# Optimization experiments

Hardware: AMD Instinct MI355X
Metric: run time of the kernel (lower is better)

Reference implementation:

```python
import jax, jax.numpy as jnp
import numpy as np

N, E, IN, H, OUT = 50000, 1600000, 128, 128, 16


def setup_inputs() -> dict:
    key = jax.random.key(0)
    ks = jax.random.split(key, 8)
    return {
        "x": jax.random.normal(ks[0], (N, IN), dtype=jnp.float32),
        "edge_index": jax.random.randint(ks[1], (2, E), 0, N, dtype=jnp.int64),
        "W1": jax.random.normal(ks[2], (IN, H), dtype=jnp.float32) * 0.05,
        "b1": jax.random.normal(ks[3], (H,), dtype=jnp.float32) * 0.05,
        "W2": jax.random.normal(ks[4], (H, H), dtype=jnp.float32) * 0.05,
        "b2": jax.random.normal(ks[5], (H,), dtype=jnp.float32) * 0.05,
        "Wc": jax.random.normal(ks[6], (H, OUT), dtype=jnp.float32) * 0.05,
        "bc": jax.random.normal(ks[7], (OUT,), dtype=jnp.float32) * 0.05,
    }


def _gcn_conv(x, src, dst, norm, W, b, n):
    # PyG GCNConv: h = x @ W; out[i] = sum_{(j->i)} norm_e * h[j]; out += b
    h = x @ W
    msg = h[src] * norm[:, None]          # [E+N, H] gather + scale
    out = jax.ops.segment_sum(msg, dst, num_segments=n)  # scatter-add
    return out + b


def reference(x, edge_index, W1, b1, W2, b2, Wc, bc):
    n = x.shape[0]
    loop = jnp.arange(n, dtype=edge_index.dtype)
    src = jnp.concatenate([edge_index[0], loop])  # add self-loops
    dst = jnp.concatenate([edge_index[1], loop])
    # symmetric normalization: deg over destinations (incl. self-loops)
    deg = jnp.zeros((n,), dtype=x.dtype).at[dst].add(1.0)
    d_inv_sqrt = jnp.where(deg > 0, jax.lax.rsqrt(deg), 0.0)
    norm = d_inv_sqrt[src] * d_inv_sqrt[dst]
    h = jax.nn.relu(_gcn_conv(x, src, dst, norm, W1, b1, n))
    # dropout p=0.5 is identity in eval mode
    h = jax.nn.relu(_gcn_conv(h, src, dst, norm, W2, b2, n))
    return h @ Wc + bc
```

## Files before the change

### kernel.cpp

```cpp
#include <hip/hip_runtime.h>
#include <hip/hip_bf16.h>


typedef unsigned int uint;
typedef unsigned short ushort;
typedef __attribute__((ext_vector_type(8))) short bf16x8;
typedef __attribute__((ext_vector_type(4))) float f32x4;

#define NPB 256
#define MAXBKT 256
#define CAP 12288

static __device__ __forceinline__ ushort f2bf(float f) {
    unsigned u = __float_as_uint(f);
    u += 0x7fffu + ((u >> 16) & 1u);
    return (ushort)(u >> 16);
}
static __device__ __forceinline__ uint pack2(float a, float b) {
    return (uint)f2bf(a) | ((uint)f2bf(b) << 16);
}
static __device__ __forceinline__ float lo2f(uint u) { return __uint_as_float(u << 16); }
static __device__ __forceinline__ float hi2f(uint u) { return __uint_as_float(u & 0xffff0000u); }

#define UNPACK8(dst, u)                                        \
    dst[0] = lo2f(u.x); dst[1] = hi2f(u.x);                    \
    dst[2] = lo2f(u.y); dst[3] = hi2f(u.y);                    \
    dst[4] = lo2f(u.z); dst[5] = hi2f(u.z);                    \
    dst[6] = lo2f(u.w); dst[7] = hi2f(u.w);


__global__ __launch_bounds__(256) void initcur(int* __restrict__ bcursor, int nbuckets) {
    int t = threadIdx.x;
    if (t < nbuckets) bcursor[t] = t * CAP;
}

__global__ __launch_bounds__(256) void bin_edges(const int* __restrict__ src,
                                                 const int* __restrict__ dst,
                                                 int* __restrict__ bcursor,
                                                 uint* __restrict__ pay,
                                                 int E, int nbuckets) {
    __shared__ int h[MAXBKT];
    __shared__ int base[MAXBKT];
    int tid = threadIdx.x;
    h[tid] = 0;
    __syncthreads();
    int chunk = (E + gridDim.x - 1) / gridDim.x;
    int i0 = blockIdx.x * chunk;
    int i1 = min(E, i0 + chunk);
    for (int i = i0 + tid; i < i1; i += 256) atomicAdd(&h[dst[i] >> 8], 1);
    __syncthreads();
    if (tid < nbuckets) base[tid] = h[tid] ? atomicAdd(&bcursor[tid], h[tid]) : 0;
    __syncthreads();
    h[tid] = 0;
    __syncthreads();
    for (int i = i0 + tid; i < i1; i += 256) {
        int d = dst[i];
        int b = d >> 8;
        int pos = base[b] + atomicAdd(&h[b], 1);
        pay[pos] = (uint)src[i] | ((uint)(d & 255) << 24);
    }
}

__global__ __launch_bounds__(256) void build_rows(const uint* __restrict__ pay,
                                                  const int* __restrict__ bcursor,
                                                  int* __restrict__ rowstart,
                                                  int* __restrict__ rowend,
                                                  float* __restrict__ dinv,
                                                  int* __restrict__ colidx, int n) {
    __shared__ int hist[NPB];
    __shared__ int sc[NPB];
    __shared__ int cur[NPB];
    int tid = threadIdx.x;
    int b = blockIdx.x;
    int node0 = b * NPB;
    int s = b * CAP, e = bcursor[b];

    hist[tid] = 0;
    __syncthreads();
    for (int i = s + tid; i < e; i += 256) atomicAdd(&hist[pay[i] >> 24], 1);
    __syncthreads();

    int v = hist[tid];
    sc[tid] = v;
    __syncthreads();
    for (int d = 1; d < 256; d <<= 1) {
        int x = (tid >= d) ? sc[tid - d] : 0;
        __syncthreads();
        sc[tid] += x;
        __syncthreads();
    }
    int excl = sc[tid] - v;
    cur[tid] = s + excl;
    int node = node0 + tid;
    if (node < n) {
        rowstart[node] = s + excl;
        rowend[node] = s + excl + v;
        dinv[node] = rsqrtf((float)(v + 1));
    }
    __syncthreads();

    for (int i = s + tid; i < e; i += 256) {
        uint p = pay[i];
        int pos = atomicAdd(&cur[p >> 24], 1);
        colidx[pos] = (int)(p & 0xffffffu);
    }
}

__global__ __launch_bounds__(256) void prep_wt(const float* __restrict__ W1,
                                               const float* __restrict__ W2,
                                               ushort* __restrict__ Wt1,
                                               ushort* __restrict__ Wt2) {
    int idx = blockIdx.x * 256 + threadIdx.x;
    int k = idx >> 7, nn = idx & 127;
    Wt1[nn * 128 + k] = f2bf(W1[idx]);
    Wt2[nn * 128 + k] = f2bf(W2[idx]);
}

template <bool A_BF16>
__global__ __launch_bounds__(256) void gemm_mfma(const void* __restrict__ Xv,
                                                 const ushort* __restrict__ Wt,
                                                 const float* __restrict__ dinv,
                                                 uint* __restrict__ Yb, int n) {
    __shared__ __align__(16) ushort sOut[4][16][136];
    const int wave = threadIdx.x >> 6;
    const int lane = threadIdx.x & 63;
    const int quad = lane >> 4, l16 = lane & 15;
    const int m0 = blockIdx.x * 64 + wave * 16;

    f32x4 acc[8];
#pragma unroll
    for (int t = 0; t < 8; ++t) acc[t] = (f32x4){0.f, 0.f, 0.f, 0.f};

    int arow = m0 + l16;
    arow = arow < n ? arow : n - 1;

#pragma unroll
    for (int ks = 0; ks < 4; ++ks) {
        bf16x8 a;
        if (A_BF16) {
            const ushort* X = (const ushort*)Xv;
            a = *(const bf16x8*)&X[(size_t)arow * 128 + ks * 32 + quad * 8];
        } else {
            const float* X = (const float*)Xv;
            const float* px = &X[(size_t)arow * 128 + ks * 32 + quad * 8];
            float4 x0 = *(const float4*)px;
            float4 x1 = *(const float4*)(px + 4);
            ushort av[8] = {f2bf(x0.x), f2bf(x0.y), f2bf(x0.z), f2bf(x0.w),
                            f2bf(x1.x), f2bf(x1.y), f2bf(x1.z), f2bf(x1.w)};
            a = *(const bf16x8*)av;
        }
#pragma unroll
        for (int nt = 0; nt < 8; ++nt) {
            bf16x8 b = *(const bf16x8*)&Wt[(size_t)(nt * 16 + l16) * 128 + ks * 32 + quad * 8];
            acc[nt] = __builtin_amdgcn_mfma_f32_16x16x32_bf16(a, b, acc[nt], 0, 0, 0);
        }
    }

    float dv[4];
#pragma unroll
    for (int r = 0; r < 4; ++r) {
        int rr = m0 + quad * 4 + r;
        dv[r] = dinv[rr < n ? rr : n - 1];
    }
#pragma unroll
    for (int nt = 0; nt < 8; ++nt)
#pragma unroll
        for (int r = 0; r < 4; ++r)
            sOut[wave][quad * 4 + r][nt * 16 + l16] = f2bf(acc[nt][r] * dv[r]);
    __syncthreads();

#pragma unroll
    for (int i = 0; i < 4; ++i) {
        int linear = i * 64 + lane;
        int row = linear >> 4, chunk = linear & 15;
        int rr = m0 + row;
        if (rr < n) {
            uint4 v = *(const uint4*)&sOut[wave][row][chunk * 8];
            *(uint4*)&Yb[(size_t)rr * 64 + chunk * 4] = v;
        }
    }
}

static __device__ __forceinline__ void gather_q(const uint4* __restrict__ H4,
                                                int s, int e, int nn, int sub,
                                                const int* __restrict__ colidx,
                                                float acc[8]) {
    uint4 su = H4[(size_t)nn * 16 + sub];
    float t[8];
    UNPACK8(t, su);
#pragma unroll
    for (int j = 0; j < 8; ++j) acc[j] = t[j];

    int p = s;
    for (; p + 8 <= e; p += 8) {
        int c[8];
#pragma unroll
        for (int i = 0; i < 8; ++i) c[i] = colidx[p + i];
        uint4 u[8];
#pragma unroll
        for (int i = 0; i < 8; ++i) u[i] = H4[(size_t)c[i] * 16 + sub];
#pragma unroll
        for (int i = 0; i < 8; ++i) {
            float a[8];
            UNPACK8(a, u[i]);
#pragma unroll
            for (int j = 0; j < 8; ++j) acc[j] += a[j];
        }
    }
    if (p < e) {
        int c[8];
#pragma unroll
        for (int i = 0; i < 8; ++i) c[i] = (p + i < e) ? colidx[p + i] : nn;
        uint4 u[8];
#pragma unroll
        for (int i = 0; i < 8; ++i) u[i] = H4[(size_t)c[i] * 16 + sub];
#pragma unroll
        for (int i = 0; i < 8; ++i) {
            float a[8];
            UNPACK8(a, u[i]);
#pragma unroll
            for (int j = 0; j < 8; ++j) acc[j] += a[j];
        }
        float pad = (float)(p + 8 - e);
#pragma unroll
        for (int j = 0; j < 8; ++j) acc[j] -= pad * t[j];
    }
}

__global__ __launch_bounds__(256) void agg_mid_q(const uint4* __restrict__ H4,
                                                 const int* __restrict__ rowstart,
                                                 const int* __restrict__ rowend,
                                                 const int* __restrict__ colidx,
                                                 const float* __restrict__ dinv,
                                                 const float* __restrict__ bias,
                                                 uint4* __restrict__ Ob, int n) {
    int tid = threadIdx.x;
    int sub = tid & 15;
    int node = blockIdx.x * 16 + (tid >> 4);
    int nn = node < n ? node : n - 1;
    int s = rowstart[nn], e = rowend[nn];
    float di = dinv[nn];

    float acc[8];
    gather_q(H4, s, e, nn, sub, colidx, acc);

    if (node < n) {
        float4 b0 = ((const float4*)bias)[sub * 2];
        float4 b1 = ((const float4*)bias)[sub * 2 + 1];
        float o0 = fmaxf(fmaf(acc[0], di, b0.x), 0.f);
        float o1 = fmaxf(fmaf(acc[1], di, b0.y), 0.f);
        float o2 = fmaxf(fmaf(acc[2], di, b0.z), 0.f);
        float o3 = fmaxf(fmaf(acc[3], di, b0.w), 0.f);
        float o4 = fmaxf(fmaf(acc[4], di, b1.x), 0.f);
        float o5 = fmaxf(fmaf(acc[5], di, b1.y), 0.f);
        float o6 = fmaxf(fmaf(acc[6], di, b1.z), 0.f);
        float o7 = fmaxf(fmaf(acc[7], di, b1.w), 0.f);
        uint4 ov;
        ov.x = pack2(o0, o1); ov.y = pack2(o2, o3);
        ov.z = pack2(o4, o5); ov.w = pack2(o6, o7);
        Ob[(size_t)node * 16 + sub] = ov;
    }
}

__global__ __launch_bounds__(256) void agg_out_q(const uint4* __restrict__ H4,
                                                 const int* __restrict__ rowstart,
                                                 const int* __restrict__ rowend,
                                                 const int* __restrict__ colidx,
                                                 const float* __restrict__ dinv,
                                                 const float* __restrict__ bias,
                                                 const float* __restrict__ Wc,
                                                 const float* __restrict__ bc,
                                                 float* __restrict__ out, int n) {
    __shared__ float sA[16][129];
    int tid = threadIdx.x;
    int sub = tid & 15;
    int nl = tid >> 4;
    int node = blockIdx.x * 16 + nl;
    int nn = node < n ? node : n - 1;
    int s = rowstart[nn], e = rowend[nn];
    float di = dinv[nn];

    float acc[8];
    gather_q(H4, s, e, nn, sub, colidx, acc);

    {
        float4 b0 = ((const float4*)bias)[sub * 2];
        float4 b1 = ((const float4*)bias)[sub * 2 + 1];
        float f[8];
        f[0] = fmaxf(fmaf(acc[0], di, b0.x), 0.f);
        f[1] = fmaxf(fmaf(acc[1], di, b0.y), 0.f);
        f[2] = fmaxf(fmaf(acc[2], di, b0.z), 0.f);
        f[3] = fmaxf(fmaf(acc[3], di, b0.w), 0.f);
        f[4] = fmaxf(fmaf(acc[4], di, b1.x), 0.f);
        f[5] = fmaxf(fmaf(acc[5], di, b1.y), 0.f);
        f[6] = fmaxf(fmaf(acc[6], di, b1.z), 0.f);
        f[7] = fmaxf(fmaf(acc[7], di, b1.w), 0.f);
#pragma unroll
        for (int j = 0; j < 8; ++j) sA[nl][sub * 8 + j] = f[j];
    }
    __syncthreads();

    int col = tid & 15;
    float p0 = 0.f, p1 = 0.f;
#pragma unroll 4
    for (int k = 0; k < 128; k += 2) {
        p0 = fmaf(sA[nl][k], Wc[k * 16 + col], p0);
        p1 = fmaf(sA[nl][k + 1], Wc[(k + 1) * 16 + col], p1);
    }
    if (node < n) out[(size_t)node * 16 + col] = p0 + p1 + bc[col];
}


extern "C" void kernel_launch(void* const* d_in, const int* in_sizes, int n_in,
                              void* d_out, int out_size, void* d_ws, size_t ws_size,
                              hipStream_t stream) {
    const float* x  = (const float*)d_in[0];
    const int*   ei = (const int*)d_in[1];
    const float* W1 = (const float*)d_in[2];
    const float* b1 = (const float*)d_in[3];
    const float* W2 = (const float*)d_in[4];
    const float* b2 = (const float*)d_in[5];
    const float* Wc = (const float*)d_in[6];
    const float* bc = (const float*)d_in[7];
    float* out = (float*)d_out;

    const int n = in_sizes[0] / 128;
    const int E = in_sizes[1] / 2;
    const int* src = ei;
    const int* dst = ei + E;
    const int nbuckets = (n + NPB - 1) / NPB;

    char* p = (char*)d_ws;
    auto alloc = [&](size_t bytes) {
        char* q = p;
        p += (bytes + 255) & ~(size_t)255;
        return q;
    };
    int*    bcursor  = (int*)alloc(MAXBKT * 4);
    int*    rowstart = (int*)alloc((size_t)n * 4);
    int*    rowend   = (int*)alloc((size_t)n * 4);
    float*  dinv     = (float*)alloc((size_t)n * 4);
    ushort* Wt1      = (ushort*)alloc(128 * 128 * 2);
    ushort* Wt2      = (ushort*)alloc(128 * 128 * 2);
    uint*   pay      = (uint*)alloc((size_t)nbuckets * CAP * 4);
    int*    colidx   = (int*)alloc((size_t)nbuckets * CAP * 4);
    uint*   bufA     = (uint*)alloc((size_t)n * 64 * 4);
    uint*   bufB     = (uint*)alloc((size_t)n * 64 * 4);
    if ((size_t)(p - (char*)d_ws) > ws_size) return;

    initcur<<<1, 256, 0, stream>>>(bcursor, nbuckets);
    bin_edges<<<256, 256, 0, stream>>>(src, dst, bcursor, pay, E, nbuckets);
    build_rows<<<nbuckets, 256, 0, stream>>>(pay, bcursor, rowstart, rowend, dinv, colidx, n);
    prep_wt<<<64, 256, 0, stream>>>(W1, W2, Wt1, Wt2);

    const int gemmb = (n + 63) / 64;
    const int aggb = (n + 15) / 16;
    gemm_mfma<false><<<gemmb, 256, 0, stream>>>(x, Wt1, dinv, bufA, n);
    agg_mid_q<<<aggb, 256, 0, stream>>>((const uint4*)bufA, rowstart, rowend, colidx,
                                        dinv, b1, (uint4*)bufB, n);
    gemm_mfma<true><<<gemmb, 256, 0, stream>>>(bufB, Wt2, dinv, bufA, n);
    agg_out_q<<<aggb, 256, 0, stream>>>((const uint4*)bufA, rowstart, rowend, colidx,
                                        dinv, b2, Wc, bc, out, n);
}
```

Measured before the change: 284.2 us.

## Store hidden features feature-group-major and shrink column indices to 16 bits

Intermediate bf16 feature buffers change from node-major rows to 16 feature-group planes of 16 bytes per node. Each aggregation block now covers 128 nodes for two feature groups, so the randomly gathered working set per block is a single small plane that stays cache-resident. Column indices are stored as 16-bit values, which halves index traffic but only holds while the node count fits in 16 bits. The final layer's 128x16 projection is split across the 8 feature-group blocks and combined with float atomics into a zeroed output, which adds a memset and many atomics.

```diff
diff --git a/kernel.cpp b/kernel.cpp
--- a/kernel.cpp
+++ b/kernel.cpp
@@ -66,7 +66,7 @@
                                                   int* __restrict__ rowstart,
                                                   int* __restrict__ rowend,
                                                   float* __restrict__ dinv,
-                                                  int* __restrict__ colidx, int n) {
+                                                  ushort* __restrict__ colidx, int n) {
     __shared__ int hist[NPB];
     __shared__ int sc[NPB];
     __shared__ int cur[NPB];
@@ -102,7 +102,7 @@
     for (int i = s + tid; i < e; i += 256) {
         uint p = pay[i];
         int pos = atomicAdd(&cur[p >> 24], 1);
-        colidx[pos] = (int)(p & 0xffffffu);
+        colidx[pos] = (ushort)p;
     }
 }
 
@@ -139,7 +139,7 @@
         bf16x8 a;
         if (A_BF16) {
             const ushort* X = (const ushort*)Xv;
-            a = *(const bf16x8*)&X[(size_t)arow * 128 + ks * 32 + quad * 8];
+            a = *(const bf16x8*)&X[((size_t)(ks * 4 + quad) * n + arow) * 8];
         } else {
             const float* X = (const float*)Xv;
             const float* px = &X[(size_t)arow * 128 + ks * 32 + quad * 8];
@@ -172,20 +172,20 @@
 #pragma unroll
     for (int i = 0; i < 4; ++i) {
         int linear = i * 64 + lane;
-        int row = linear >> 4, chunk = linear & 15;
+        int g = linear >> 4, row = linear & 15;
         int rr = m0 + row;
         if (rr < n) {
-            uint4 v = *(const uint4*)&sOut[wave][row][chunk * 8];
-            *(uint4*)&Yb[(size_t)rr * 64 + chunk * 4] = v;
-        }
-    }
-}
-
-static __device__ __forceinline__ void gather_q(const uint4* __restrict__ H4,
-                                                int s, int e, int nn, int sub,
-                                                const int* __restrict__ colidx,
+            uint4 v = *(const uint4*)&sOut[wave][row][g * 8];
+            *(uint4*)&Yb[((size_t)g * n + rr) * 4] = v;
+        }
+    }
+}
+
+static __device__ __forceinline__ void gather_g(const uint4* __restrict__ Hg,
+                                                int s, int e, int nn, size_t gbase,
+                                                const ushort* __restrict__ colidx,
                                                 float acc[8]) {
-    uint4 su = H4[(size_t)nn * 16 + sub];
+    uint4 su = Hg[gbase + nn];
     float t[8];
     UNPACK8(t, su);
 #pragma unroll
@@ -198,7 +198,7 @@
         for (int i = 0; i < 8; ++i) c[i] = colidx[p + i];
         uint4 u[8];
 #pragma unroll
-        for (int i = 0; i < 8; ++i) u[i] = H4[(size_t)c[i] * 16 + sub];
+        for (int i = 0; i < 8; ++i) u[i] = Hg[gbase + c[i]];
 #pragma unroll
         for (int i = 0; i < 8; ++i) {
             float a[8];
@@ -210,10 +210,10 @@
     if (p < e) {
         int c[8];
 #pragma unroll
-        for (int i = 0; i < 8; ++i) c[i] = (p + i < e) ? colidx[p + i] : nn;
+        for (int i = 0; i < 8; ++i) c[i] = (p + i < e) ? (int)colidx[p + i] : nn;
         uint4 u[8];
 #pragma unroll
-        for (int i = 0; i < 8; ++i) u[i] = H4[(size_t)c[i] * 16 + sub];
+        for (int i = 0; i < 8; ++i) u[i] = Hg[gbase + c[i]];
 #pragma unroll
         for (int i = 0; i < 8; ++i) {
             float a[8];
@@ -227,26 +227,30 @@
     }
 }
 
-__global__ __launch_bounds__(256) void agg_mid_q(const uint4* __restrict__ H4,
+__global__ __launch_bounds__(256) void agg_mid_c(const uint4* __restrict__ Hg,
                                                  const int* __restrict__ rowstart,
                                                  const int* __restrict__ rowend,
-                                                 const int* __restrict__ colidx,
+                                                 const ushort* __restrict__ colidx,
                                                  const float* __restrict__ dinv,
                                                  const float* __restrict__ bias,
-                                                 uint4* __restrict__ Ob, int n) {
+                                                 uint4* __restrict__ Og, int n) {
     int tid = threadIdx.x;
-    int sub = tid & 15;
-    int node = blockIdx.x * 16 + (tid >> 4);
+    int sub = tid & 1;
+    int f = blockIdx.x & 7;
+    int node = (blockIdx.x >> 3) * 128 + (tid >> 1);
     int nn = node < n ? node : n - 1;
     int s = rowstart[nn], e = rowend[nn];
     float di = dinv[nn];
+    int g = f * 2 + sub;
+    size_t gbase = (size_t)g * n;
 
     float acc[8];
-    gather_q(H4, s, e, nn, sub, colidx, acc);
+    gather_g(Hg, s, e, nn, gbase, colidx, acc);
 
     if (node < n) {
-        float4 b0 = ((const float4*)bias)[sub * 2];
-        float4 b1 = ((const float4*)bias)[sub * 2 + 1];
+        const float4* B4 = (const float4*)bias;
+        float4 b0 = B4[g * 2];
+        float4 b1 = B4[g * 2 + 1];
         float o0 = fmaxf(fmaf(acc[0], di, b0.x), 0.f);
         float o1 = fmaxf(fmaf(acc[1], di, b0.y), 0.f);
         float o2 = fmaxf(fmaf(acc[2], di, b0.z), 0.f);
@@ -258,56 +262,76 @@
         uint4 ov;
         ov.x = pack2(o0, o1); ov.y = pack2(o2, o3);
         ov.z = pack2(o4, o5); ov.w = pack2(o6, o7);
-        Ob[(size_t)node * 16 + sub] = ov;
-    }
-}
-
-__global__ __launch_bounds__(256) void agg_out_q(const uint4* __restrict__ H4,
+        Og[gbase + node] = ov;
+    }
+}
+
+__global__ __launch_bounds__(256) void agg_fin_c(const uint4* __restrict__ Hg,
                                                  const int* __restrict__ rowstart,
                                                  const int* __restrict__ rowend,
-                                                 const int* __restrict__ colidx,
+                                                 const ushort* __restrict__ colidx,
                                                  const float* __restrict__ dinv,
                                                  const float* __restrict__ bias,
                                                  const float* __restrict__ Wc,
                                                  const float* __restrict__ bc,
                                                  float* __restrict__ out, int n) {
-    __shared__ float sA[16][129];
     int tid = threadIdx.x;
-    int sub = tid & 15;
-    int nl = tid >> 4;
-    int node = blockIdx.x * 16 + nl;
+    int sub = tid & 1;
+    int f = blockIdx.x & 7;
+    int node = (blockIdx.x >> 3) * 128 + (tid >> 1);
     int nn = node < n ? node : n - 1;
     int s = rowstart[nn], e = rowend[nn];
     float di = dinv[nn];
+    int g = f * 2 + sub;
+    size_t gbase = (size_t)g * n;
 
     float acc[8];
-    gather_q(H4, s, e, nn, sub, colidx, acc);
-
+    gather_g(Hg, s, e, nn, gbase, colidx, acc);
+
+    float a[8];
     {
-        float4 b0 = ((const float4*)bias)[sub * 2];
-        float4 b1 = ((const float4*)bias)[sub * 2 + 1];
-        float f[8];
-        f[0] = fmaxf(fmaf(acc[0], di, b0.x), 0.f);
-        f[1] = fmaxf(fmaf(acc[1], di, b0.y), 0.f);
-        f[2] = fmaxf(fmaf(acc[2], di, b0.z), 0.f);
-        f[3] = fmaxf(fmaf(acc[3], di, b0.w), 0.f);
-        f[4] = fmaxf(fmaf(acc[4], di, b1.x), 0.f);
-        f[5] = fmaxf(fmaf(acc[5], di, b1.y), 0.f);
-        f[6] = fmaxf(fmaf(acc[6], di, b1.z), 0.f);
-        f[7] = fmaxf(fmaf(acc[7], di, b1.w), 0.f);
-#pragma unroll
-        for (int j = 0; j < 8; ++j) sA[nl][sub * 8 + j] = f[j];
-    }
-    __syncthreads();
-
-    int col = tid & 15;
-    float p0 = 0.f, p1 = 0.f;
-#pragma unroll 4
-    for (int k = 0; k < 128; k += 2) {
-        p0 = fmaf(sA[nl][k], Wc[k * 16 + col], p0);
-        p1 = fmaf(sA[nl][k + 1], Wc[(k + 1) * 16 + col], p1);
-    }
-    if (node < n) out[(size_t)node * 16 + col] = p0 + p1 + bc[col];
+        const float4* B4 = (const float4*)bias;
+        float4 b0 = B4[g * 2];
+        float4 b1 = B4[g * 2 + 1];
+        a[0] = fmaxf(fmaf(acc[0], di, b0.x), 0.f);
+        a[1] = fmaxf(fmaf(acc[1], di, b0.y), 0.f);
+        a[2] = fmaxf(fmaf(acc[2], di, b0.z), 0.f);
+        a[3] = fmaxf(fmaf(acc[3], di, b0.w), 0.f);
+        a[4] = fmaxf(fmaf(acc[4], di, b1.x), 0.f);
+        a[5] = fmaxf(fmaf(acc[5], di, b1.y), 0.f);
+        a[6] = fmaxf(fmaf(acc[6], di, b1.z), 0.f);
+        a[7] = fmaxf(fmaf(acc[7], di, b1.w), 0.f);
+    }
+
+    float p[16];
+#pragma unroll
+    for (int c = 0; c < 16; ++c) p[c] = 0.f;
+#pragma unroll
+    for (int j = 0; j < 8; ++j) {
+        const float4* wr = (const float4*)&Wc[(size_t)(g * 8 + j) * 16];
+        float4 w0 = wr[0], w1 = wr[1], w2 = wr[2], w3 = wr[3];
+        float aj = a[j];
+        p[0]  = fmaf(aj, w0.x, p[0]);  p[1]  = fmaf(aj, w0.y, p[1]);
+        p[2]  = fmaf(aj, w0.z, p[2]);  p[3]  = fmaf(aj, w0.w, p[3]);
+        p[4]  = fmaf(aj, w1.x, p[4]);  p[5]  = fmaf(aj, w1.y, p[5]);
+        p[6]  = fmaf(aj, w1.z, p[6]);  p[7]  = fmaf(aj, w1.w, p[7]);
+        p[8]  = fmaf(aj, w2.x, p[8]);  p[9]  = fmaf(aj, w2.y, p[9]);
+        p[10] = fmaf(aj, w2.z, p[10]); p[11] = fmaf(aj, w2.w, p[11]);
+        p[12] = fmaf(aj, w3.x, p[12]); p[13] = fmaf(aj, w3.y, p[13]);
+        p[14] = fmaf(aj, w3.z, p[14]); p[15] = fmaf(aj, w3.w, p[15]);
+    }
+#pragma unroll
+    for (int c = 0; c < 16; ++c) p[c] += __shfl_xor(p[c], 1);
+
+    if (node < n) {
+        int cb = sub * 8;
+#pragma unroll
+        for (int k = 0; k < 8; ++k) {
+            float v = p[cb + k];
+            if (f == 0) v += bc[cb + k];
+            atomicAdd(&out[(size_t)node * 16 + cb + k], v);
+        }
+    }
 }
 
 
@@ -343,10 +367,12 @@
     ushort* Wt1      = (ushort*)alloc(128 * 128 * 2);
     ushort* Wt2      = (ushort*)alloc(128 * 128 * 2);
     uint*   pay      = (uint*)alloc((size_t)nbuckets * CAP * 4);
-    int*    colidx   = (int*)alloc((size_t)nbuckets * CAP * 4);
+    ushort* colidx   = (ushort*)alloc((size_t)nbuckets * CAP * 2);
     uint*   bufA     = (uint*)alloc((size_t)n * 64 * 4);
     uint*   bufB     = (uint*)alloc((size_t)n * 64 * 4);
     if ((size_t)(p - (char*)d_ws) > ws_size) return;
+
+    hipMemsetAsync(out, 0, (size_t)n * 16 * sizeof(float), stream);
 
     initcur<<<1, 256, 0, stream>>>(bcursor, nbuckets);
     bin_edges<<<256, 256, 0, stream>>>(src, dst, bcursor, pay, E, nbuckets);
@@ -354,11 +380,11 @@
     prep_wt<<<64, 256, 0, stream>>>(W1, W2, Wt1, Wt2);
 
     const int gemmb = (n + 63) / 64;
-    const int aggb = (n + 15) / 16;
+    const int aggb = 8 * ((n + 127) / 128);
     gemm_mfma<false><<<gemmb, 256, 0, stream>>>(x, Wt1, dinv, bufA, n);
-    agg_mid_q<<<aggb, 256, 0, stream>>>((const uint4*)bufA, rowstart, rowend, colidx,
+    agg_mid_c<<<aggb, 256, 0, stream>>>((const uint4*)bufA, rowstart, rowend, colidx,
                                         dinv, b1, (uint4*)bufB, n);
     gemm_mfma<true><<<gemmb, 256, 0, stream>>>(bufB, Wt2, dinv, bufA, n);
-    agg_out_q<<<aggb, 256, 0, stream>>>((const uint4*)bufA, rowstart, rowend, colidx,
+    agg_fin_c<<<aggb, 256, 0, stream>>>((const uint4*)bufA, rowstart, rowend, colidx,
                                         dinv, b2, Wc, bc, out, n);
 }
```

Measured after the change: 484.8 us. 1.71x slower.

## Store CSR column indices as 16-bit and sub-sort row neighbors by source range

Applied to the files above, without the earlier changes.

Column indices are stored as ushort instead of int, halving the index traffic read by both aggregation kernels. build_rows also orders each row's neighbors by which quarter of the node range the source falls in, to improve cache locality of the feature gathers. The bin_edges grid grows from 256 to 1024 blocks. Sixteen-bit indices only hold when the node count stays below 65536, and the per-row quarter histogram adds shared-memory atomics and an integer division per edge.

```diff
diff --git a/kernel.cpp b/kernel.cpp
--- a/kernel.cpp
+++ b/kernel.cpp
@@ -9,6 +9,7 @@
 
 #define NPB 256
 #define MAXBKT 256
+#define NQ 4
 #define CAP 12288
 
 static __device__ __forceinline__ ushort f2bf(float f) {
@@ -66,22 +67,28 @@
                                                   int* __restrict__ rowstart,
                                                   int* __restrict__ rowend,
                                                   float* __restrict__ dinv,
-                                                  int* __restrict__ colidx, int n) {
-    __shared__ int hist[NPB];
+                                                  ushort* __restrict__ colidx, int n) {
+    __shared__ int hist[NPB * NQ];
     __shared__ int sc[NPB];
-    __shared__ int cur[NPB];
+    __shared__ int cur[NPB * NQ];
     int tid = threadIdx.x;
     int b = blockIdx.x;
     int node0 = b * NPB;
     int s = b * CAP, e = bcursor[b];
-
-    hist[tid] = 0;
-    __syncthreads();
-    for (int i = s + tid; i < e; i += 256) atomicAdd(&hist[pay[i] >> 24], 1);
-    __syncthreads();
-
-    int v = hist[tid];
-    sc[tid] = v;
+    int qsize = (n + NQ - 1) / NQ;
+
+    for (int i = tid; i < NPB * NQ; i += 256) hist[i] = 0;
+    __syncthreads();
+    for (int i = s + tid; i < e; i += 256) {
+        uint p = pay[i];
+        atomicAdd(&hist[(int)(p >> 24) * NQ + (int)(p & 0xffffffu) / qsize], 1);
+    }
+    __syncthreads();
+
+    int h0 = hist[tid * NQ], h1 = hist[tid * NQ + 1];
+    int h2 = hist[tid * NQ + 2], h3 = hist[tid * NQ + 3];
+    int tot = h0 + h1 + h2 + h3;
+    sc[tid] = tot;
     __syncthreads();
     for (int d = 1; d < 256; d <<= 1) {
         int x = (tid >= d) ? sc[tid - d] : 0;
@@ -89,20 +96,24 @@
         sc[tid] += x;
         __syncthreads();
     }
-    int excl = sc[tid] - v;
-    cur[tid] = s + excl;
+    int excl = sc[tid] - tot;
+    cur[tid * NQ]     = s + excl;
+    cur[tid * NQ + 1] = s + excl + h0;
+    cur[tid * NQ + 2] = s + excl + h0 + h1;
+    cur[tid * NQ + 3] = s + excl + h0 + h1 + h2;
     int node = node0 + tid;
     if (node < n) {
         rowstart[node] = s + excl;
-        rowend[node] = s + excl + v;
-        dinv[node] = rsqrtf((float)(v + 1));
+        rowend[node] = s + excl + tot;
+        dinv[node] = rsqrtf((float)(tot + 1));
     }
     __syncthreads();
 
     for (int i = s + tid; i < e; i += 256) {
         uint p = pay[i];
-        int pos = atomicAdd(&cur[p >> 24], 1);
-        colidx[pos] = (int)(p & 0xffffffu);
+        int srcv = (int)(p & 0xffffffu);
+        int pos = atomicAdd(&cur[(int)(p >> 24) * NQ + srcv / qsize], 1);
+        colidx[pos] = (ushort)srcv;
     }
 }
 
@@ -183,7 +194,7 @@
 
 static __device__ __forceinline__ void gather_q(const uint4* __restrict__ H4,
                                                 int s, int e, int nn, int sub,
-                                                const int* __restrict__ colidx,
+                                                const ushort* __restrict__ colidx,
                                                 float acc[8]) {
     uint4 su = H4[(size_t)nn * 16 + sub];
     float t[8];
@@ -210,7 +221,7 @@
     if (p < e) {
         int c[8];
 #pragma unroll
-        for (int i = 0; i < 8; ++i) c[i] = (p + i < e) ? colidx[p + i] : nn;
+        for (int i = 0; i < 8; ++i) c[i] = (p + i < e) ? (int)colidx[p + i] : nn;
         uint4 u[8];
 #pragma unroll
         for (int i = 0; i < 8; ++i) u[i] = H4[(size_t)c[i] * 16 + sub];
@@ -230,7 +241,7 @@
 __global__ __launch_bounds__(256) void agg_mid_q(const uint4* __restrict__ H4,
                                                  const int* __restrict__ rowstart,
                                                  const int* __restrict__ rowend,
-                                                 const int* __restrict__ colidx,
+                                                 const ushort* __restrict__ colidx,
                                                  const float* __restrict__ dinv,
                                                  const float* __restrict__ bias,
                                                  uint4* __restrict__ Ob, int n) {
@@ -265,7 +276,7 @@
 __global__ __launch_bounds__(256) void agg_out_q(const uint4* __restrict__ H4,
                                                  const int* __restrict__ rowstart,
                                                  const int* __restrict__ rowend,
-                                                 const int* __restrict__ colidx,
+                                                 const ushort* __restrict__ colidx,
                                                  const float* __restrict__ dinv,
                                                  const float* __restrict__ bias,
                                                  const float* __restrict__ Wc,
@@ -343,13 +354,13 @@
     ushort* Wt1      = (ushort*)alloc(128 * 128 * 2);
     ushort* Wt2      = (ushort*)alloc(128 * 128 * 2);
     uint*   pay      = (uint*)alloc((size_t)nbuckets * CAP * 4);
-    int*    colidx   = (int*)alloc((size_t)nbuckets * CAP * 4);
+    ushort* colidx   = (ushort*)alloc((size_t)nbuckets * CAP * 2);
     uint*   bufA     = (uint*)alloc((size_t)n * 64 * 4);
     uint*   bufB     = (uint*)alloc((size_t)n * 64 * 4);
     if ((size_t)(p - (char*)d_ws) > ws_size) return;
 
     initcur<<<1, 256, 0, stream>>>(bcursor, nbuckets);
-    bin_edges<<<256, 256, 0, stream>>>(src, dst, bcursor, pay, E, nbuckets);
+    bin_edges<<<1024, 256, 0, stream>>>(src, dst, bcursor, pay, E, nbuckets);
     build_rows<<<nbuckets, 256, 0, stream>>>(pay, bcursor, rowstart, rowend, dinv, colidx, n);
     prep_wt<<<64, 256, 0, stream>>>(W1, W2, Wt1, Wt2);
 
```

Result: no change. 284.8 us (+0.2%).
